# Kernel optimization log

Measured on AMD Instinct MI355X. Metric: run time of the kernel, lower is better.

## Reference

```python
import jax, jax.numpy as jnp
import numpy as np

H, DH = 16, 64            # heads, dim_head (rope dim == DH)
NUM_CHAINS = 2
TWO_PI = 2.0 * np.pi
LN_EPS = 1e-5


def layer_norm(x, gamma):
    mu = jnp.mean(x, axis=-1, keepdims=True)
    var = jnp.var(x, axis=-1, keepdims=True)
    return (x - mu) * jax.lax.rsqrt(var + LN_EPS) * gamma


def rotate_half(x):
    # pairs are interleaved: (..., d*2) viewed as (..., d, 2); (x1,x2)->(-x2,x1)
    x1 = x[..., 0::2]
    x2 = x[..., 1::2]
    return jnp.stack((-x2, x1), axis=-1).reshape(x.shape)


def cyclic_rope_freqs(residue_index, chain_index, cyclic_mask, rope_freqs, dtype):
    """Angles [B,L,DH]: standard RoPE (with chain-offset combination) for linear
    tokens, ring harmonics omega_i = 2*pi*k_i/L_chain for cyclic tokens."""
    t = residue_index.astype(dtype)                      # B L (interpolate_factor=1)
    ci = chain_index.astype(dtype)
    F = rope_freqs.shape[0]                              # DH//2 = 32
    # standard path (RotaryEmbedding._forward with chain_index):
    # residue_indices = arange(F)%F = identity; chain_indices = arange(F)//F = 0
    res = t[..., None] * rope_freqs                      # B L F
    ch0 = ci * rope_freqs[0]                             # B L  (chain_freqs[...,0])
    std = jnp.repeat(res + ch0[..., None], 2, axis=-1)   # B L DH (interleaved repeat)
    # ring size per token: count of cyclic tokens on each token's chain
    oh = jax.nn.one_hot(chain_index, NUM_CHAINS, dtype=dtype)        # B L C
    counts = jnp.einsum('blc,bl->bc', oh, cyclic_mask)               # B C
    ring = jnp.take_along_axis(counts, chain_index, axis=1) * cyclic_mask  # B L
    ring_safe = jnp.maximum(ring, 1.0)
    max_k = jnp.maximum(jnp.floor(ring_safe * 0.5), 1.0)             # B L
    kk = jnp.arange(1, F + 1, dtype=dtype)
    k_eff = jnp.where(max_k[..., None] == 1.0, 1.0,
                      1.0 + jnp.mod(kk - 1.0, max_k[..., None]))     # B L F
    omega = TWO_PI * k_eff / ring_safe[..., None]                    # B L F
    cyc = jnp.repeat(omega * t[..., None], 2, axis=-1)               # B L DH
    return jnp.where((cyclic_mask > 0)[..., None], cyc, std)


def setup_inputs() -> dict:
    key = jax.random.key(0)
    ks = jax.random.split(key, 8)
    B, L, dim = 4, 1024, 1024
    s = 0.02
    x = jax.random.normal(ks[0], (B, L, dim), jnp.float32)
    time = jax.random.normal(ks[1], (B, 1, dim), jnp.float32)
    seq_mask = jnp.ones((B, L), jnp.float32)
    residue_index = (jnp.arange(B * L, dtype=jnp.int32).reshape(B, L)) % L
    chain_index = jax.random.randint(ks[2], (B, L), 0, NUM_CHAINS).astype(jnp.int32)
    cyclic_mask = jax.random.randint(ks[3], (B, L), 0, 2).astype(jnp.float32)
    gamma = jnp.ones((dim,), jnp.float32)
    Wt = jax.random.normal(ks[4], (2 * dim, dim), jnp.float32) * s
    bt = jnp.zeros((2 * dim,), jnp.float32)
    Wq = jax.random.normal(ks[5], (H * DH, dim), jnp.float32) * s
    Wkv = jax.random.normal(ks[6], (2 * H * DH, dim), jnp.float32) * s
    Wo = jax.random.normal(ks[7], (dim, H * DH), jnp.float32) * s
    rope_freqs = 1.0 / (10000.0 ** (jnp.arange(0, DH, 2, dtype=jnp.float32) / DH))
    return {"x": x, "time": time, "seq_mask": seq_mask, "cyclic_mask": cyclic_mask,
            "gamma": gamma, "Wt": Wt, "bt": bt, "Wq": Wq, "Wkv": Wkv, "Wo": Wo,
            "rope_freqs": rope_freqs,
            "residue_index": residue_index, "chain_index": chain_index}


def reference(x, time, seq_mask, cyclic_mask, gamma, Wt, bt, Wq, Wkv, Wo,
              rope_freqs, residue_index, chain_index):
    B, L, dim = x.shape
    x = x * seq_mask[..., None]
    xn = layer_norm(x, gamma)
    # time conditioning: SiLU -> Linear -> (scale, shift)
    ss = jax.nn.silu(time) @ Wt.T + bt                   # B 1 2*dim
    scale, shift = jnp.split(ss, 2, axis=-1)
    xc = xn * (scale + 1.0) + shift                      # B L dim
    q = (xc @ Wq.T).reshape(B, L, H, DH).transpose(0, 2, 1, 3)   # B H L Dh
    k, v = jnp.split(xc @ Wkv.T, 2, axis=-1)
    k = k.reshape(B, L, H, DH).transpose(0, 2, 1, 3)
    v = v.reshape(B, L, H, DH).transpose(0, 2, 1, 3)
    # cyclic rotary embeddings (full head dim rotated)
    freqs = cyclic_rope_freqs(residue_index, chain_index, cyclic_mask,
                              rope_freqs, x.dtype)        # B L DH
    cos_f = jnp.cos(freqs)[:, None]                       # B 1 L DH
    sin_f = jnp.sin(freqs)[:, None]
    q = q * cos_f + rotate_half(q) * sin_f
    k = k * cos_f + rotate_half(k) * sin_f
    sim = jnp.einsum('bhid,bhjd->bhij', q * (DH ** -0.5), k)
    neg = -jnp.finfo(sim.dtype).max
    sim = jnp.where(seq_mask[:, None, None, :] > 0, sim, neg)
    attn = jax.nn.softmax(sim, axis=-1)
    out = jnp.einsum('bhij,bhjd->bhid', attn, v)
    out = out.transpose(0, 2, 1, 3).reshape(B, L, H * DH)
    out = out @ Wo.T
    return out * seq_mask[..., None]
```

## Files before the change

kernel.cpp:

```cpp
#include <hip/hip_runtime.h>
#include <hip/hip_bf16.h>
#include <math.h>

#define NB 4
#define NL 1024
#define NDIM 1024
#define NH 16
#define NDH 64
#define NEG_MAX (-3.402823466e38f)

typedef __attribute__((ext_vector_type(4))) float fx4;
typedef __attribute__((ext_vector_type(8))) short bh8;

__device__ __forceinline__ ushort f2bf(float f){
    __hip_bfloat16 h = __float2bfloat16(f);
    return *(ushort*)&h;
}
__device__ __forceinline__ float bf2f(ushort h){
    return __uint_as_float(((unsigned)h)<<16);
}
__device__ __forceinline__ void gload16(const void* g, void* l){
    __builtin_amdgcn_global_load_lds((const __attribute__((address_space(1))) void*)g,
                                     (__attribute__((address_space(3))) void*)l, 16, 0, 0);
}

__global__ __launch_bounds__(256) void k_ss(const float* __restrict__ time_, const float* __restrict__ Wt,
                                            const float* __restrict__ bt, float* __restrict__ ss){
    int gw   = (blockIdx.x*256 + threadIdx.x) >> 6;
    int lane = threadIdx.x & 63;
    int b = gw >> 11, j = gw & 2047;
    const float* a = time_ + b*NDIM;
    const float* w = Wt + (size_t)j*NDIM;
    float s = 0.f;
    #pragma unroll 4
    for (int i = lane; i < NDIM; i += 64){
        float v = a[i];
        s += (v / (1.f + __expf(-v))) * w[i];
    }
    #pragma unroll
    for (int off=32; off; off>>=1) s += __shfl_xor(s, off, 64);
    if (!lane) ss[gw] = s + bt[j];
}

__global__ __launch_bounds__(256) void k_counts(const int* __restrict__ chain, const float* __restrict__ cyc,
                                                float* __restrict__ counts){
    int b = blockIdx.x >> 1, c = blockIdx.x & 1;
    float s = 0.f;
    for (int l = threadIdx.x; l < NL; l += 256)
        s += (chain[b*NL+l]==c) ? cyc[b*NL+l] : 0.f;
    __shared__ float red[4];
    #pragma unroll
    for (int off=32; off; off>>=1) s += __shfl_xor(s, off, 64);
    if (!(threadIdx.x & 63)) red[threadIdx.x>>6] = s;
    __syncthreads();
    if (!threadIdx.x) counts[blockIdx.x] = red[0]+red[1]+red[2]+red[3];
}

__global__ __launch_bounds__(256) void k_angles(const int* __restrict__ resi, const int* __restrict__ chain,
                                                const float* __restrict__ cyc, const float* __restrict__ rf,
                                                const float* __restrict__ counts,
                                                float* __restrict__ cosb, float* __restrict__ sinb){
    int idx = blockIdx.x*256 + threadIdx.x;
    int f  = idx & 31;
    int bl = idx >> 5;
    int b  = bl >> 10;
    float t  = (float)resi[bl];
    int   ci = chain[bl];
    float cm = cyc[bl];
    float ang;
    if (cm > 0.f) {
        float ring      = counts[b*2+ci] * cm;
        float ring_safe = fmaxf(ring, 1.f);
        float max_k     = fmaxf(floorf(ring_safe*0.5f), 1.f);
        float k_eff     = (max_k == 1.f) ? 1.f : (1.f + fmodf((float)f, max_k));
        float omega     = 6.28318530717958647692f * k_eff / ring_safe;
        ang = omega * t;
    } else {
        ang = t * rf[f] + (float)ci * rf[0];
    }
    cosb[idx] = cosf(ang);
    sinb[idx] = sinf(ang);
}

__global__ __launch_bounds__(256) void k_convall(const float* __restrict__ Wq, const float* __restrict__ Wkv,
                                                 const float* __restrict__ Wo,
                                                 ushort* __restrict__ wqkv, ushort* __restrict__ wo){
    int i = (blockIdx.x*256 + threadIdx.x)*4;
    if (i >= 4194304) return;
    const float* src; ushort* dst;
    if (i < 3145728){
        dst = wqkv + i;
        src = (i < 1048576) ? (Wq + i) : (Wkv + (i - 1048576));
    } else {
        dst = wo + (i - 3145728);
        src = Wo + (i - 3145728);
    }
    fx4 v = *(const fx4*)src;
    ushort4 o; o.x=f2bf(v.x); o.y=f2bf(v.y); o.z=f2bf(v.z); o.w=f2bf(v.w);
    *(ushort4*)dst = o;
}

__global__ __launch_bounds__(256) void k_lnmod(const float* __restrict__ x, const float* __restrict__ sm,
                                               const float* __restrict__ gamma, const float* __restrict__ ss,
                                               ushort* __restrict__ xc){
    int row = blockIdx.x;
    int b   = row >> 10;
    int t   = threadIdx.x;
    float msk = sm[row];
    fx4 v = ((const fx4*)(x + (size_t)row*NDIM))[t];
    v.x*=msk; v.y*=msk; v.z*=msk; v.w*=msk;
    float s1 = v.x+v.y+v.z+v.w;
    float s2 = v.x*v.x + v.y*v.y + v.z*v.z + v.w*v.w;
    __shared__ float r1[4], r2[4];
    #pragma unroll
    for (int off=32; off; off>>=1){ s1 += __shfl_xor(s1,off,64); s2 += __shfl_xor(s2,off,64); }
    if (!(t & 63)){ r1[t>>6]=s1; r2[t>>6]=s2; }
    __syncthreads();
    s1 = r1[0]+r1[1]+r1[2]+r1[3];
    s2 = r2[0]+r2[1]+r2[2]+r2[3];
    float mu  = s1 * (1.f/NDIM);
    float var = s2 * (1.f/NDIM) - mu*mu;
    float rs  = rsqrtf(var + 1e-5f);
    const float* sc = ss + b*2048;
    fx4 g   = ((const fx4*)gamma)[t];
    fx4 scl = ((const fx4*)sc)[t];
    fx4 sh  = ((const fx4*)(sc+1024))[t];
    ushort4 ob;
    ob.x = f2bf((v.x-mu)*rs*g.x*(1.f+scl.x)+sh.x);
    ob.y = f2bf((v.y-mu)*rs*g.y*(1.f+scl.y)+sh.y);
    ob.z = f2bf((v.z-mu)*rs*g.z*(1.f+scl.z)+sh.z);
    ob.w = f2bf((v.w-mu)*rs*g.w*(1.f+scl.w)+sh.w);
    *(ushort4*)(xc + (size_t)row*NDIM + t*4) = ob;
}

template<int MODE>
__global__ __launch_bounds__(256) void k_mm(const ushort* __restrict__ A, const ushort* __restrict__ W,
                                            ushort* __restrict__ qo, ushort* __restrict__ ko,
                                            ushort* __restrict__ vo,
                                            float* __restrict__ outf, const float* __restrict__ smask){
    __shared__ ushort As[128*32];
    __shared__ ushort Bs[128*32];
    int t = threadIdx.x, l = t&63, w = t>>6;
    int lo = l&15, hi = l>>4;
    int m0 = blockIdx.y*128, n0 = blockIdx.x*128;
    int wm = (w>>1)*64, wn = (w&1)*64;
    fx4 acc[4][4];
    #pragma unroll
    for (int i=0;i<4;i++)
        #pragma unroll
        for (int j=0;j<4;j++) acc[i][j] = (fx4){0.f,0.f,0.f,0.f};
    const char* Ab = (const char*)A;
    const char* Wb = (const char*)W;
    for (int k0=0; k0<NDIM; k0+=32){
        __syncthreads();
        #pragma unroll
        for (int e=0;e<2;e++){
            int c = t + e*256;
            int row = c>>2, cw = c&3;
            gload16(Ab + (size_t)(m0+row)*2048 + k0*2 + cw*16, (char*)As + c*16);
            gload16(Wb + (size_t)(n0+row)*2048 + k0*2 + cw*16, (char*)Bs + c*16);
        }
        __syncthreads();
        bh8 af[4], bf[4];
        #pragma unroll
        for (int i=0;i<4;i++) af[i] = *(const bh8*)(As + (wm + i*16 + lo)*32 + hi*8);
        #pragma unroll
        for (int j=0;j<4;j++) bf[j] = *(const bh8*)(Bs + (wn + j*16 + lo)*32 + hi*8);
        #pragma unroll
        for (int i=0;i<4;i++)
            #pragma unroll
            for (int j=0;j<4;j++)
                acc[i][j] = __builtin_amdgcn_mfma_f32_16x16x32_bf16(af[i], bf[j], acc[i][j], 0, 0, 0);
    }
    #pragma unroll
    for (int i=0;i<4;i++){
        #pragma unroll
        for (int r=0;r<4;r++){
            int m = m0 + wm + i*16 + hi*4 + r;
            int b_ = m>>10, l_ = m&1023;
            #pragma unroll
            for (int j=0;j<4;j++){
                int n = n0 + wn + j*16 + lo;
                float val = acc[i][j][r];
                if (MODE==0){
                    int nn = n & 1023;
                    int h_ = nn>>6, d_ = nn&63;
                    size_t off = (size_t)((b_*NH + h_)*NL + l_)*NDH + d_;
                    if (n < 1024)      qo[off] = f2bf(val);
                    else if (n < 2048) ko[off] = f2bf(val);
                    else               vo[off] = f2bf(val);
                } else {
                    outf[(size_t)m*NDIM + n] = val * smask[m];
                }
            }
        }
    }
}

__global__ __launch_bounds__(256) void k_rope(ushort* __restrict__ q, ushort* __restrict__ k,
                                              const float* __restrict__ cosb, const float* __restrict__ sinb){
    int idx = blockIdx.x*256 + threadIdx.x;
    int f   = idx & 31;
    int bhl = idx >> 5;
    int l   = bhl & 1023;
    int b   = bhl >> 14;
    int ca  = ((b<<10)|l)*32 + f;
    float c = cosb[ca], s = sinb[ca];
    const float QS = 0.18033688011112042f;
    unsigned qp = ((const unsigned*)q)[idx];
    unsigned kp = ((const unsigned*)k)[idx];
    float qx = bf2f((ushort)(qp&0xffffu)), qy = bf2f((ushort)(qp>>16));
    float kx = bf2f((ushort)(kp&0xffffu)), ky = bf2f((ushort)(kp>>16));
    float q0 = (qx*c - qy*s)*QS, q1 = (qy*c + qx*s)*QS;
    float k0 = kx*c - ky*s,      k1 = ky*c + kx*s;
    ((unsigned*)q)[idx] = (unsigned)f2bf(q0) | ((unsigned)f2bf(q1)<<16);
    ((unsigned*)k)[idx] = (unsigned)f2bf(k0) | ((unsigned)f2bf(k1)<<16);
}

__global__ __launch_bounds__(256) void k_vt(const ushort* __restrict__ v, ushort* __restrict__ vt){
    __shared__ ushort tile[64][65];
    int t = threadIdx.x;
    int bh = blockIdx.y, l0 = blockIdx.x*64;
    #pragma unroll
    for (int e=0;e<2;e++){
        int c = t + e*256;
        int row = c>>3, cw = c&7;
        bh8 d = *(const bh8*)(v + ((size_t)bh*NL + l0 + row)*NDH + cw*8);
        #pragma unroll
        for (int x=0;x<8;x++) tile[row][cw*8+x] = (ushort)d[x];
    }
    __syncthreads();
    #pragma unroll
    for (int e=0;e<2;e++){
        int c = t + e*256;
        int drow = c>>3, cw = c&7;
        bh8 o;
        #pragma unroll
        for (int x=0;x<8;x++) o[x] = (short)tile[cw*8+x][drow];
        *(bh8*)(vt + ((size_t)bh*NDH + drow)*NL + l0 + cw*8) = o;
    }
}

__global__ __launch_bounds__(256) void k_fattn(const ushort* __restrict__ qb, const ushort* __restrict__ kb,
                                               const ushort* __restrict__ vt, const float* __restrict__ smask,
                                               ushort* __restrict__ ao){
    __shared__ ushort Ks[2][64*64];
    __shared__ ushort Vs[2][64*64];
    __shared__ ushort Ps[4][32*64];
    int t = threadIdx.x, l = t&63, w = t>>6;
    int lo = l&15, hi = l>>4;
    int logical = (blockIdx.x & 7)*64 + (blockIdx.x >> 3);
    int bh = logical >> 3;
    int qt = logical & 7;
    int b = bh>>4, h = bh&15;
    int q0 = qt*128;
    int swzq = (lo&7)<<4;

    bh8 aq[2][2];
    #pragma unroll
    for (int qs=0; qs<2; qs++){
        const ushort* qrow = qb + ((size_t)bh*NL + q0 + w*32 + qs*16 + lo)*NDH;
        aq[qs][0] = *(const bh8*)(qrow + hi*8);
        aq[qs][1] = *(const bh8*)(qrow + 32 + hi*8);
    }
    const float* mrow = smask + b*NL;

    fx4 o[2][4];
    float mrun[2], lrun[2];
    #pragma unroll
    for (int qs=0; qs<2; qs++){
        mrun[qs]=NEG_MAX; lrun[qs]=0.f;
        #pragma unroll
        for (int dt=0; dt<4; dt++) o[qs][dt] = (fx4){0.f,0.f,0.f,0.f};
    }

    const char* kbase = (const char*)(kb + (size_t)bh*NL*NDH);
    const char* vbase = (const char*)(vt + (size_t)bh*NDH*NL);

    #define STAGE(bb, jt) { \
        int j0s = (jt)*64; \
        _Pragma("unroll") \
        for (int e=0;e<2;e++){ \
            int c = t + e*256; \
            int row = c>>3, cw = c&7; \
            int lc = cw ^ (row&7); \
            gload16(kbase + (size_t)(j0s+row)*128 + lc*16, (char*)Ks[bb] + c*16); \
        } \
        _Pragma("unroll") \
        for (int e=0;e<2;e++){ \
            int c = t + e*256; \
            int row = c>>3, cw = c&7; \
            int lc = cw ^ (row&7); \
            gload16(vbase + (size_t)row*2048 + j0s*2 + lc*16, (char*)Vs[bb] + c*16); \
        } }

    STAGE(0, 0);
    __syncthreads();

    for (int tt=0; tt<16; ++tt){
        int cur = tt & 1;
        if (tt < 15) STAGE(cur^1, tt+1);
        int j0 = tt*64;
        const char* KsB = (const char*)Ks[cur];
        const char* VsB = (const char*)Vs[cur];
        char* PsB = (char*)&Ps[w][0];

        bh8 kf[4][2];
        #pragma unroll
        for (int j=0;j<4;j++){
            int row = j*16 + lo;
            int swz = (row&7)<<4;
            kf[j][0] = *(const bh8*)(KsB + row*128 + ((hi*16) ^ swz));
            kf[j][1] = *(const bh8*)(KsB + row*128 + ((64 + hi*16) ^ swz));
        }
        fx4 s[2][4];
        #pragma unroll
        for (int qs=0; qs<2; qs++)
            #pragma unroll
            for (int j=0;j<4;j++){
                fx4 z = (fx4){0.f,0.f,0.f,0.f};
                z = __builtin_amdgcn_mfma_f32_16x16x32_bf16(kf[j][0], aq[qs][0], z, 0,0,0);
                z = __builtin_amdgcn_mfma_f32_16x16x32_bf16(kf[j][1], aq[qs][1], z, 0,0,0);
                s[qs][j] = z;
            }
        #pragma unroll
        for (int j=0;j<4;j++){
            float4 mv = *(const float4*)(mrow + j0 + j*16 + hi*4);
            s[0][j][0] = mv.x>0.f ? s[0][j][0] : NEG_MAX;  s[1][j][0] = mv.x>0.f ? s[1][j][0] : NEG_MAX;
            s[0][j][1] = mv.y>0.f ? s[0][j][1] : NEG_MAX;  s[1][j][1] = mv.y>0.f ? s[1][j][1] : NEG_MAX;
            s[0][j][2] = mv.z>0.f ? s[0][j][2] : NEG_MAX;  s[1][j][2] = mv.z>0.f ? s[1][j][2] : NEG_MAX;
            s[0][j][3] = mv.w>0.f ? s[0][j][3] : NEG_MAX;  s[1][j][3] = mv.w>0.f ? s[1][j][3] : NEG_MAX;
        }

        #pragma unroll
        for (int qs=0; qs<2; qs++){
            float mt = s[qs][0][0];
            #pragma unroll
            for (int j=0;j<4;j++)
                #pragma unroll
                for (int r=0;r<4;r++) mt = fmaxf(mt, s[qs][j][r]);
            mt = fmaxf(mt, __shfl_xor(mt, 16));
            mt = fmaxf(mt, __shfl_xor(mt, 32));
            float mnew = fmaxf(mrun[qs], mt);
            float cc = __builtin_amdgcn_exp2f(mrun[qs] - mnew);
            float p[4][4];
            float rs = 0.f;
            #pragma unroll
            for (int j=0;j<4;j++)
                #pragma unroll
                for (int r=0;r<4;r++){ p[j][r] = __builtin_amdgcn_exp2f(s[qs][j][r] - mnew); rs += p[j][r]; }
            rs += __shfl_xor(rs, 16);
            rs += __shfl_xor(rs, 32);
            lrun[qs] = lrun[qs]*cc + rs;
            mrun[qs] = mnew;
            #pragma unroll
            for (int r=0;r<4;r++){
                float ccr = __shfl(cc, hi*4 + r);
                #pragma unroll
                for (int dt=0; dt<4; dt++) o[qs][dt][r] *= ccr;
            }
            #pragma unroll
            for (int j=0;j<4;j++)
                #pragma unroll
                for (int pp=0; pp<2; pp++){
                    unsigned word = (unsigned)f2bf(p[j][2*pp]) | ((unsigned)f2bf(p[j][2*pp+1])<<16);
                    int kv0 = j*16 + hi*4 + 2*pp;
                    *(unsigned*)(PsB + (qs*16+lo)*128 + ((kv0*2) ^ swzq)) = word;
                }
        }

        bh8 ap[2][2];
        #pragma unroll
        for (int qs=0; qs<2; qs++){
            ap[qs][0] = *(const bh8*)(PsB + (qs*16+lo)*128 + ((hi*16) ^ swzq));
            ap[qs][1] = *(const bh8*)(PsB + (qs*16+lo)*128 + ((64 + hi*16) ^ swzq));
        }
        #pragma unroll
        for (int dt=0; dt<4; dt++){
            int row = dt*16 + lo;
            int swz = (row&7)<<4;
            bh8 bv0 = *(const bh8*)(VsB + row*128 + ((hi*16) ^ swz));
            bh8 bv1 = *(const bh8*)(VsB + row*128 + ((64 + hi*16) ^ swz));
            o[0][dt] = __builtin_amdgcn_mfma_f32_16x16x32_bf16(ap[0][0], bv0, o[0][dt], 0,0,0);
            o[0][dt] = __builtin_amdgcn_mfma_f32_16x16x32_bf16(ap[0][1], bv1, o[0][dt], 0,0,0);
            o[1][dt] = __builtin_amdgcn_mfma_f32_16x16x32_bf16(ap[1][0], bv0, o[1][dt], 0,0,0);
            o[1][dt] = __builtin_amdgcn_mfma_f32_16x16x32_bf16(ap[1][1], bv1, o[1][dt], 0,0,0);
        }
        __syncthreads();
    }
    #undef STAGE

    #pragma unroll
    for (int qs=0; qs<2; qs++){
        float inv = 1.f / lrun[qs];
        #pragma unroll
        for (int r=0;r<4;r++){
            float ivr = __shfl(inv, hi*4 + r);
            int l_ = q0 + w*32 + qs*16 + hi*4 + r;
            size_t base = ((size_t)b*NL + l_)*NDIM + h*NDH;
            #pragma unroll
            for (int dt=0; dt<4; dt++)
                ao[base + dt*16 + lo] = f2bf(o[qs][dt][r] * ivr);
        }
    }
}

extern "C" void kernel_launch(void* const* d_in, const int* in_sizes, int n_in,
                              void* d_out, int out_size, void* d_ws, size_t ws_size,
                              hipStream_t stream) {
    const float* x      = (const float*)d_in[0];
    const float* time_  = (const float*)d_in[1];
    const float* smask  = (const float*)d_in[2];
    const float* cycm   = (const float*)d_in[3];
    const float* gamma  = (const float*)d_in[4];
    const float* Wt     = (const float*)d_in[5];
    const float* bt     = (const float*)d_in[6];
    const float* Wq     = (const float*)d_in[7];
    const float* Wkv    = (const float*)d_in[8];
    const float* Wo     = (const float*)d_in[9];
    const float* rf     = (const float*)d_in[10];
    const int*   resi   = (const int*)d_in[11];
    const int*   chain  = (const int*)d_in[12];
    float* out = (float*)d_out;

    float*  ss     = (float*)d_ws;
    float*  cnts   = ss + 8192;
    float*  cosb   = cnts + 16;
    float*  sinb   = cosb + 131072;
    ushort* xc     = (ushort*)(sinb + 131072);
    ushort* wqkv   = xc + 4194304;
    ushort* wo     = wqkv + 3145728;
    ushort* qbuf   = wo + 1048576;
    ushort* kbuf   = qbuf + 4194304;
    ushort* vbuf   = kbuf + 4194304;
    ushort* vtb    = vbuf + 4194304;
    ushort* aob    = vtb + 4194304;

    hipLaunchKernelGGL(k_ss,      dim3(2048),    dim3(256), 0, stream, time_, Wt, bt, ss);
    hipLaunchKernelGGL(k_counts,  dim3(8),       dim3(256), 0, stream, chain, cycm, cnts);
    hipLaunchKernelGGL(k_angles,  dim3(512),     dim3(256), 0, stream, resi, chain, cycm, rf, cnts, cosb, sinb);
    hipLaunchKernelGGL(k_convall, dim3(4096),    dim3(256), 0, stream, Wq, Wkv, Wo, wqkv, wo);
    hipLaunchKernelGGL(k_lnmod,   dim3(4096),    dim3(256), 0, stream, x, smask, gamma, ss, xc);
    hipLaunchKernelGGL((k_mm<0>), dim3(24,32),   dim3(256), 0, stream, xc, wqkv, qbuf, kbuf, vbuf, (float*)nullptr, (const float*)nullptr);
    hipLaunchKernelGGL(k_rope,    dim3(8192),    dim3(256), 0, stream, qbuf, kbuf, cosb, sinb);
    hipLaunchKernelGGL(k_vt,      dim3(16,64),   dim3(256), 0, stream, vbuf, vtb);
    hipLaunchKernelGGL(k_fattn,   dim3(512),     dim3(256), 0, stream, qbuf, kbuf, vtb, smask, aob);
    hipLaunchKernelGGL((k_mm<1>), dim3(8,32),    dim3(256), 0, stream, aob, wo, (ushort*)nullptr, (ushort*)nullptr, (ushort*)nullptr, out, smask);
}
```

Before: 230.7 us.

## Merge prep kernels, double-buffer GEMM, swizzle tiles, lazy softmax rescale in attention

```diff
diff --git a/kernel.cpp b/kernel.cpp
--- a/kernel.cpp
+++ b/kernel.cpp
@@ -24,113 +24,115 @@
                                      (__attribute__((address_space(3))) void*)l, 16, 0, 0);
 }
 
-__global__ __launch_bounds__(256) void k_ss(const float* __restrict__ time_, const float* __restrict__ Wt,
-                                            const float* __restrict__ bt, float* __restrict__ ss){
-    int gw   = (blockIdx.x*256 + threadIdx.x) >> 6;
-    int lane = threadIdx.x & 63;
-    int b = gw >> 11, j = gw & 2047;
-    const float* a = time_ + b*NDIM;
-    const float* w = Wt + (size_t)j*NDIM;
-    float s = 0.f;
-    #pragma unroll 4
-    for (int i = lane; i < NDIM; i += 64){
-        float v = a[i];
-        s += (v / (1.f + __expf(-v))) * w[i];
-    }
-    #pragma unroll
-    for (int off=32; off; off>>=1) s += __shfl_xor(s, off, 64);
-    if (!lane) ss[gw] = s + bt[j];
-}
-
-__global__ __launch_bounds__(256) void k_counts(const int* __restrict__ chain, const float* __restrict__ cyc,
-                                                float* __restrict__ counts){
-    int b = blockIdx.x >> 1, c = blockIdx.x & 1;
-    float s = 0.f;
-    for (int l = threadIdx.x; l < NL; l += 256)
-        s += (chain[b*NL+l]==c) ? cyc[b*NL+l] : 0.f;
+__global__ __launch_bounds__(256) void k_pre1(const float* __restrict__ time_, const float* __restrict__ Wt,
+                                              const float* __restrict__ bt, float* __restrict__ ss,
+                                              const int* __restrict__ chain, const float* __restrict__ cyc,
+                                              float* __restrict__ counts,
+                                              const float* __restrict__ Wq, const float* __restrict__ Wkv,
+                                              const float* __restrict__ Wo,
+                                              ushort* __restrict__ wqkv, ushort* __restrict__ wo){
     __shared__ float red[4];
-    #pragma unroll
-    for (int off=32; off; off>>=1) s += __shfl_xor(s, off, 64);
-    if (!(threadIdx.x & 63)) red[threadIdx.x>>6] = s;
-    __syncthreads();
-    if (!threadIdx.x) counts[blockIdx.x] = red[0]+red[1]+red[2]+red[3];
-}
-
-__global__ __launch_bounds__(256) void k_angles(const int* __restrict__ resi, const int* __restrict__ chain,
-                                                const float* __restrict__ cyc, const float* __restrict__ rf,
-                                                const float* __restrict__ counts,
-                                                float* __restrict__ cosb, float* __restrict__ sinb){
-    int idx = blockIdx.x*256 + threadIdx.x;
-    int f  = idx & 31;
-    int bl = idx >> 5;
-    int b  = bl >> 10;
-    float t  = (float)resi[bl];
-    int   ci = chain[bl];
-    float cm = cyc[bl];
-    float ang;
-    if (cm > 0.f) {
-        float ring      = counts[b*2+ci] * cm;
-        float ring_safe = fmaxf(ring, 1.f);
-        float max_k     = fmaxf(floorf(ring_safe*0.5f), 1.f);
-        float k_eff     = (max_k == 1.f) ? 1.f : (1.f + fmodf((float)f, max_k));
-        float omega     = 6.28318530717958647692f * k_eff / ring_safe;
-        ang = omega * t;
+    int bx = blockIdx.x, t = threadIdx.x;
+    if (bx < 2048){
+        int gw   = (bx*256 + t) >> 6;
+        int lane = t & 63;
+        int b = gw >> 11, j = gw & 2047;
+        const float* a = time_ + b*NDIM;
+        const float* w = Wt + (size_t)j*NDIM;
+        float s = 0.f;
+        #pragma unroll 4
+        for (int i = lane; i < NDIM; i += 64){
+            float v = a[i];
+            s += (v / (1.f + __expf(-v))) * w[i];
+        }
+        #pragma unroll
+        for (int off=32; off; off>>=1) s += __shfl_xor(s, off, 64);
+        if (!lane) ss[gw] = s + bt[j];
+    } else if (bx < 2056){
+        int cb = bx - 2048;
+        int b = cb >> 1, c = cb & 1;
+        float s = 0.f;
+        for (int l = t; l < NL; l += 256)
+            s += (chain[b*NL+l]==c) ? cyc[b*NL+l] : 0.f;
+        #pragma unroll
+        for (int off=32; off; off>>=1) s += __shfl_xor(s, off, 64);
+        if (!(t & 63)) red[t>>6] = s;
+        __syncthreads();
+        if (!t) counts[cb] = red[0]+red[1]+red[2]+red[3];
     } else {
-        ang = t * rf[f] + (float)ci * rf[0];
-    }
-    cosb[idx] = cosf(ang);
-    sinb[idx] = sinf(ang);
-}
-
-__global__ __launch_bounds__(256) void k_convall(const float* __restrict__ Wq, const float* __restrict__ Wkv,
-                                                 const float* __restrict__ Wo,
-                                                 ushort* __restrict__ wqkv, ushort* __restrict__ wo){
-    int i = (blockIdx.x*256 + threadIdx.x)*4;
-    if (i >= 4194304) return;
-    const float* src; ushort* dst;
-    if (i < 3145728){
-        dst = wqkv + i;
-        src = (i < 1048576) ? (Wq + i) : (Wkv + (i - 1048576));
+        int i = ((bx-2056)*256 + t)*4;
+        const float* src; ushort* dst;
+        if (i < 3145728){
+            dst = wqkv + i;
+            src = (i < 1048576) ? (Wq + i) : (Wkv + (i - 1048576));
+        } else {
+            dst = wo + (i - 3145728);
+            src = Wo + (i - 3145728);
+        }
+        fx4 v = *(const fx4*)src;
+        ushort4 o; o.x=f2bf(v.x); o.y=f2bf(v.y); o.z=f2bf(v.z); o.w=f2bf(v.w);
+        *(ushort4*)dst = o;
+    }
+}
+
+__global__ __launch_bounds__(256) void k_pre2(const int* __restrict__ resi, const int* __restrict__ chain,
+                                              const float* __restrict__ cyc, const float* __restrict__ rf,
+                                              const float* __restrict__ counts,
+                                              float* __restrict__ cosb, float* __restrict__ sinb,
+                                              const float* __restrict__ x, const float* __restrict__ sm,
+                                              const float* __restrict__ gamma, const float* __restrict__ ss,
+                                              ushort* __restrict__ xc){
+    __shared__ float r1[4], r2[4];
+    int bx = blockIdx.x, t = threadIdx.x;
+    if (bx < 512){
+        int idx = bx*256 + t;
+        int f  = idx & 31;
+        int bl = idx >> 5;
+        int b  = bl >> 10;
+        float tt = (float)resi[bl];
+        int   ci = chain[bl];
+        float cm = cyc[bl];
+        float ang;
+        if (cm > 0.f) {
+            float ring      = counts[b*2+ci] * cm;
+            float ring_safe = fmaxf(ring, 1.f);
+            float max_k     = fmaxf(floorf(ring_safe*0.5f), 1.f);
+            float k_eff     = (max_k == 1.f) ? 1.f : (1.f + fmodf((float)f, max_k));
+            float omega     = 6.28318530717958647692f * k_eff / ring_safe;
+            ang = omega * tt;
+        } else {
+            ang = tt * rf[f] + (float)ci * rf[0];
+        }
+        cosb[idx] = cosf(ang);
+        sinb[idx] = sinf(ang);
     } else {
-        dst = wo + (i - 3145728);
-        src = Wo + (i - 3145728);
-    }
-    fx4 v = *(const fx4*)src;
-    ushort4 o; o.x=f2bf(v.x); o.y=f2bf(v.y); o.z=f2bf(v.z); o.w=f2bf(v.w);
-    *(ushort4*)dst = o;
-}
-
-__global__ __launch_bounds__(256) void k_lnmod(const float* __restrict__ x, const float* __restrict__ sm,
-                                               const float* __restrict__ gamma, const float* __restrict__ ss,
-                                               ushort* __restrict__ xc){
-    int row = blockIdx.x;
-    int b   = row >> 10;
-    int t   = threadIdx.x;
-    float msk = sm[row];
-    fx4 v = ((const fx4*)(x + (size_t)row*NDIM))[t];
-    v.x*=msk; v.y*=msk; v.z*=msk; v.w*=msk;
-    float s1 = v.x+v.y+v.z+v.w;
-    float s2 = v.x*v.x + v.y*v.y + v.z*v.z + v.w*v.w;
-    __shared__ float r1[4], r2[4];
-    #pragma unroll
-    for (int off=32; off; off>>=1){ s1 += __shfl_xor(s1,off,64); s2 += __shfl_xor(s2,off,64); }
-    if (!(t & 63)){ r1[t>>6]=s1; r2[t>>6]=s2; }
-    __syncthreads();
-    s1 = r1[0]+r1[1]+r1[2]+r1[3];
-    s2 = r2[0]+r2[1]+r2[2]+r2[3];
-    float mu  = s1 * (1.f/NDIM);
-    float var = s2 * (1.f/NDIM) - mu*mu;
-    float rs  = rsqrtf(var + 1e-5f);
-    const float* sc = ss + b*2048;
-    fx4 g   = ((const fx4*)gamma)[t];
-    fx4 scl = ((const fx4*)sc)[t];
-    fx4 sh  = ((const fx4*)(sc+1024))[t];
-    ushort4 ob;
-    ob.x = f2bf((v.x-mu)*rs*g.x*(1.f+scl.x)+sh.x);
-    ob.y = f2bf((v.y-mu)*rs*g.y*(1.f+scl.y)+sh.y);
-    ob.z = f2bf((v.z-mu)*rs*g.z*(1.f+scl.z)+sh.z);
-    ob.w = f2bf((v.w-mu)*rs*g.w*(1.f+scl.w)+sh.w);
-    *(ushort4*)(xc + (size_t)row*NDIM + t*4) = ob;
+        int row = bx - 512;
+        int b   = row >> 10;
+        float msk = sm[row];
+        fx4 v = ((const fx4*)(x + (size_t)row*NDIM))[t];
+        v.x*=msk; v.y*=msk; v.z*=msk; v.w*=msk;
+        float s1 = v.x+v.y+v.z+v.w;
+        float s2 = v.x*v.x + v.y*v.y + v.z*v.z + v.w*v.w;
+        #pragma unroll
+        for (int off=32; off; off>>=1){ s1 += __shfl_xor(s1,off,64); s2 += __shfl_xor(s2,off,64); }
+        if (!(t & 63)){ r1[t>>6]=s1; r2[t>>6]=s2; }
+        __syncthreads();
+        s1 = r1[0]+r1[1]+r1[2]+r1[3];
+        s2 = r2[0]+r2[1]+r2[2]+r2[3];
+        float mu  = s1 * (1.f/NDIM);
+        float var = s2 * (1.f/NDIM) - mu*mu;
+        float rs  = rsqrtf(var + 1e-5f);
+        const float* sc = ss + b*2048;
+        fx4 g   = ((const fx4*)gamma)[t];
+        fx4 scl = ((const fx4*)sc)[t];
+        fx4 sh  = ((const fx4*)(sc+1024))[t];
+        ushort4 ob;
+        ob.x = f2bf((v.x-mu)*rs*g.x*(1.f+scl.x)+sh.x);
+        ob.y = f2bf((v.y-mu)*rs*g.y*(1.f+scl.y)+sh.y);
+        ob.z = f2bf((v.z-mu)*rs*g.z*(1.f+scl.z)+sh.z);
+        ob.w = f2bf((v.w-mu)*rs*g.w*(1.f+scl.w)+sh.w);
+        *(ushort4*)(xc + (size_t)row*NDIM + t*4) = ob;
+    }
 }
 
 template<int MODE>
@@ -138,11 +140,15 @@
                                             ushort* __restrict__ qo, ushort* __restrict__ ko,
                                             ushort* __restrict__ vo,
                                             float* __restrict__ outf, const float* __restrict__ smask){
-    __shared__ ushort As[128*32];
-    __shared__ ushort Bs[128*32];
+    __shared__ ushort As[2][128*32];
+    __shared__ ushort Bs[2][128*32];
     int t = threadIdx.x, l = t&63, w = t>>6;
     int lo = l&15, hi = l>>4;
-    int m0 = blockIdx.y*128, n0 = blockIdx.x*128;
+    const int nbx = (MODE==0) ? 24 : 8;
+    const int nwg = (MODE==0) ? 768 : 256;
+    int lin = blockIdx.y*nbx + blockIdx.x;
+    int swz = (lin & 7)*(nwg>>3) + (lin>>3);
+    int m0 = (swz/nbx)*128, n0 = (swz%nbx)*128;
     int wm = (w>>1)*64, wn = (w&1)*64;
     fx4 acc[4][4];
     #pragma unroll
@@ -151,27 +157,35 @@
         for (int j=0;j<4;j++) acc[i][j] = (fx4){0.f,0.f,0.f,0.f};
     const char* Ab = (const char*)A;
     const char* Wb = (const char*)W;
-    for (int k0=0; k0<NDIM; k0+=32){
-        __syncthreads();
-        #pragma unroll
-        for (int e=0;e<2;e++){
-            int c = t + e*256;
-            int row = c>>2, cw = c&3;
-            gload16(Ab + (size_t)(m0+row)*2048 + k0*2 + cw*16, (char*)As + c*16);
-            gload16(Wb + (size_t)(n0+row)*2048 + k0*2 + cw*16, (char*)Bs + c*16);
-        }
-        __syncthreads();
+
+    #define MMSTAGE(bb, k0) { \
+        _Pragma("unroll") \
+        for (int e=0;e<2;e++){ \
+            int c = t + e*256; \
+            int row = c>>2, cw = c&3; \
+            gload16(Ab + (size_t)(m0+row)*2048 + (k0)*2 + cw*16, (char*)As[bb] + c*16); \
+            gload16(Wb + (size_t)(n0+row)*2048 + (k0)*2 + cw*16, (char*)Bs[bb] + c*16); \
+        } }
+
+    MMSTAGE(0, 0);
+    __syncthreads();
+    for (int kt=0; kt<32; kt++){
+        int cur = kt & 1;
+        if (kt < 31) MMSTAGE(cur^1, (kt+1)*32);
         bh8 af[4], bf[4];
         #pragma unroll
-        for (int i=0;i<4;i++) af[i] = *(const bh8*)(As + (wm + i*16 + lo)*32 + hi*8);
-        #pragma unroll
-        for (int j=0;j<4;j++) bf[j] = *(const bh8*)(Bs + (wn + j*16 + lo)*32 + hi*8);
+        for (int i=0;i<4;i++) af[i] = *(const bh8*)(&As[cur][0] + (wm + i*16 + lo)*32 + hi*8);
+        #pragma unroll
+        for (int j=0;j<4;j++) bf[j] = *(const bh8*)(&Bs[cur][0] + (wn + j*16 + lo)*32 + hi*8);
         #pragma unroll
         for (int i=0;i<4;i++)
             #pragma unroll
             for (int j=0;j<4;j++)
                 acc[i][j] = __builtin_amdgcn_mfma_f32_16x16x32_bf16(af[i], bf[j], acc[i][j], 0, 0, 0);
-    }
+        __syncthreads();
+    }
+    #undef MMSTAGE
+
     #pragma unroll
     for (int i=0;i<4;i++){
         #pragma unroll
@@ -197,47 +211,49 @@
     }
 }
 
-__global__ __launch_bounds__(256) void k_rope(ushort* __restrict__ q, ushort* __restrict__ k,
-                                              const float* __restrict__ cosb, const float* __restrict__ sinb){
-    int idx = blockIdx.x*256 + threadIdx.x;
-    int f   = idx & 31;
-    int bhl = idx >> 5;
-    int l   = bhl & 1023;
-    int b   = bhl >> 14;
-    int ca  = ((b<<10)|l)*32 + f;
-    float c = cosb[ca], s = sinb[ca];
-    const float QS = 0.18033688011112042f;
-    unsigned qp = ((const unsigned*)q)[idx];
-    unsigned kp = ((const unsigned*)k)[idx];
-    float qx = bf2f((ushort)(qp&0xffffu)), qy = bf2f((ushort)(qp>>16));
-    float kx = bf2f((ushort)(kp&0xffffu)), ky = bf2f((ushort)(kp>>16));
-    float q0 = (qx*c - qy*s)*QS, q1 = (qy*c + qx*s)*QS;
-    float k0 = kx*c - ky*s,      k1 = ky*c + kx*s;
-    ((unsigned*)q)[idx] = (unsigned)f2bf(q0) | ((unsigned)f2bf(q1)<<16);
-    ((unsigned*)k)[idx] = (unsigned)f2bf(k0) | ((unsigned)f2bf(k1)<<16);
-}
-
-__global__ __launch_bounds__(256) void k_vt(const ushort* __restrict__ v, ushort* __restrict__ vt){
+__global__ __launch_bounds__(256) void k_mid(ushort* __restrict__ q, ushort* __restrict__ k,
+                                             const float* __restrict__ cosb, const float* __restrict__ sinb,
+                                             const ushort* __restrict__ v, ushort* __restrict__ vt){
     __shared__ ushort tile[64][65];
-    int t = threadIdx.x;
-    int bh = blockIdx.y, l0 = blockIdx.x*64;
-    #pragma unroll
-    for (int e=0;e<2;e++){
-        int c = t + e*256;
-        int row = c>>3, cw = c&7;
-        bh8 d = *(const bh8*)(v + ((size_t)bh*NL + l0 + row)*NDH + cw*8);
-        #pragma unroll
-        for (int x=0;x<8;x++) tile[row][cw*8+x] = (ushort)d[x];
-    }
-    __syncthreads();
-    #pragma unroll
-    for (int e=0;e<2;e++){
-        int c = t + e*256;
-        int drow = c>>3, cw = c&7;
-        bh8 o;
-        #pragma unroll
-        for (int x=0;x<8;x++) o[x] = (short)tile[cw*8+x][drow];
-        *(bh8*)(vt + ((size_t)bh*NDH + drow)*NL + l0 + cw*8) = o;
+    int bx = blockIdx.x, t = threadIdx.x;
+    if (bx < 8192){
+        int idx = bx*256 + t;
+        int f   = idx & 31;
+        int bhl = idx >> 5;
+        int l   = bhl & 1023;
+        int b   = bhl >> 14;
+        int ca  = ((b<<10)|l)*32 + f;
+        float c = cosb[ca], s = sinb[ca];
+        const float QS = 0.18033688011112042f;
+        unsigned qp = ((const unsigned*)q)[idx];
+        unsigned kp = ((const unsigned*)k)[idx];
+        float qx = bf2f((ushort)(qp&0xffffu)), qy = bf2f((ushort)(qp>>16));
+        float kx = bf2f((ushort)(kp&0xffffu)), ky = bf2f((ushort)(kp>>16));
+        float q0 = (qx*c - qy*s)*QS, q1 = (qy*c + qx*s)*QS;
+        float k0 = kx*c - ky*s,      k1 = ky*c + kx*s;
+        ((unsigned*)q)[idx] = (unsigned)f2bf(q0) | ((unsigned)f2bf(q1)<<16);
+        ((unsigned*)k)[idx] = (unsigned)f2bf(k0) | ((unsigned)f2bf(k1)<<16);
+    } else {
+        int vb = bx - 8192;
+        int bh = vb >> 4, l0 = (vb & 15)*64;
+        #pragma unroll
+        for (int e=0;e<2;e++){
+            int c = t + e*256;
+            int row = c>>3, cw = c&7;
+            bh8 d = *(const bh8*)(v + ((size_t)bh*NL + l0 + row)*NDH + cw*8);
+            #pragma unroll
+            for (int x2=0;x2<8;x2++) tile[row][cw*8+x2] = (ushort)d[x2];
+        }
+        __syncthreads();
+        #pragma unroll
+        for (int e=0;e<2;e++){
+            int c = t + e*256;
+            int drow = c>>3, cw = c&7;
+            bh8 o;
+            #pragma unroll
+            for (int x2=0;x2<8;x2++) o[x2] = (short)tile[cw*8+x2][drow];
+            *(bh8*)(vt + ((size_t)bh*NDH + drow)*NL + l0 + cw*8) = o;
+        }
     }
 }
 
@@ -314,6 +330,7 @@
             kf[j][1] = *(const bh8*)(KsB + row*128 + ((64 + hi*16) ^ swz));
         }
         fx4 s[2][4];
+        __builtin_amdgcn_s_setprio(1);
         #pragma unroll
         for (int qs=0; qs<2; qs++)
             #pragma unroll
@@ -323,6 +340,7 @@
                 z = __builtin_amdgcn_mfma_f32_16x16x32_bf16(kf[j][1], aq[qs][1], z, 0,0,0);
                 s[qs][j] = z;
             }
+        __builtin_amdgcn_s_setprio(0);
         #pragma unroll
         for (int j=0;j<4;j++){
             float4 mv = *(const float4*)(mrow + j0 + j*16 + hi*4);
@@ -334,39 +352,46 @@
 
         #pragma unroll
         for (int qs=0; qs<2; qs++){
-            float mt = s[qs][0][0];
+            float m0 = fmaxf(fmaxf(s[qs][0][0], s[qs][0][1]), s[qs][0][2]);
+            float m1 = fmaxf(fmaxf(s[qs][0][3], s[qs][1][0]), s[qs][1][1]);
+            float m2 = fmaxf(fmaxf(s[qs][1][2], s[qs][1][3]), s[qs][2][0]);
+            float m3 = fmaxf(fmaxf(s[qs][2][1], s[qs][2][2]), s[qs][2][3]);
+            float m4 = fmaxf(fmaxf(s[qs][3][0], s[qs][3][1]), s[qs][3][2]);
+            float mt = fmaxf(fmaxf(fmaxf(m0,m1),m2), fmaxf(fmaxf(m3,m4), s[qs][3][3]));
+            mt = fmaxf(mt, __shfl_xor(mt, 16));
+            mt = fmaxf(mt, __shfl_xor(mt, 32));
+            if (__any(mt > mrun[qs] + 8.f)){
+                float mnew = fmaxf(mrun[qs], mt);
+                float cc = __builtin_amdgcn_exp2f(mrun[qs] - mnew);
+                lrun[qs] *= cc;
+                mrun[qs] = mnew;
+                #pragma unroll
+                for (int r=0;r<4;r++){
+                    float ccr = __shfl(cc, hi*4 + r);
+                    #pragma unroll
+                    for (int dt=0; dt<4; dt++) o[qs][dt][r] *= ccr;
+                }
+            }
+            float p[4][4];
             #pragma unroll
             for (int j=0;j<4;j++)
                 #pragma unroll
-                for (int r=0;r<4;r++) mt = fmaxf(mt, s[qs][j][r]);
-            mt = fmaxf(mt, __shfl_xor(mt, 16));
-            mt = fmaxf(mt, __shfl_xor(mt, 32));
-            float mnew = fmaxf(mrun[qs], mt);
-            float cc = __builtin_amdgcn_exp2f(mrun[qs] - mnew);
-            float p[4][4];
-            float rs = 0.f;
-            #pragma unroll
-            for (int j=0;j<4;j++)
-                #pragma unroll
-                for (int r=0;r<4;r++){ p[j][r] = __builtin_amdgcn_exp2f(s[qs][j][r] - mnew); rs += p[j][r]; }
+                for (int r=0;r<4;r++) p[j][r] = __builtin_amdgcn_exp2f(s[qs][j][r] - mrun[qs]);
+            float r0 = (p[0][0]+p[0][1]) + (p[0][2]+p[0][3]);
+            float r1 = (p[1][0]+p[1][1]) + (p[1][2]+p[1][3]);
+            float r2 = (p[2][0]+p[2][1]) + (p[2][2]+p[2][3]);
+            float r3 = (p[3][0]+p[3][1]) + (p[3][2]+p[3][3]);
+            float rs = (r0+r1)+(r2+r3);
             rs += __shfl_xor(rs, 16);
             rs += __shfl_xor(rs, 32);
-            lrun[qs] = lrun[qs]*cc + rs;
-            mrun[qs] = mnew;
-            #pragma unroll
-            for (int r=0;r<4;r++){
-                float ccr = __shfl(cc, hi*4 + r);
-                #pragma unroll
-                for (int dt=0; dt<4; dt++) o[qs][dt][r] *= ccr;
+            lrun[qs] += rs;
+            #pragma unroll
+            for (int j=0;j<4;j++){
+                uint2 wd;
+                wd.x = (unsigned)f2bf(p[j][0]) | ((unsigned)f2bf(p[j][1])<<16);
+                wd.y = (unsigned)f2bf(p[j][2]) | ((unsigned)f2bf(p[j][3])<<16);
+                *(uint2*)(PsB + (qs*16+lo)*128 + ((j*32 + hi*8) ^ swzq)) = wd;
             }
-            #pragma unroll
-            for (int j=0;j<4;j++)
-                #pragma unroll
-                for (int pp=0; pp<2; pp++){
-                    unsigned word = (unsigned)f2bf(p[j][2*pp]) | ((unsigned)f2bf(p[j][2*pp+1])<<16);
-                    int kv0 = j*16 + hi*4 + 2*pp;
-                    *(unsigned*)(PsB + (qs*16+lo)*128 + ((kv0*2) ^ swzq)) = word;
-                }
         }
 
         bh8 ap[2][2];
@@ -375,6 +400,7 @@
             ap[qs][0] = *(const bh8*)(PsB + (qs*16+lo)*128 + ((hi*16) ^ swzq));
             ap[qs][1] = *(const bh8*)(PsB + (qs*16+lo)*128 + ((64 + hi*16) ^ swzq));
         }
+        __builtin_amdgcn_s_setprio(1);
         #pragma unroll
         for (int dt=0; dt<4; dt++){
             int row = dt*16 + lo;
@@ -386,6 +412,7 @@
             o[1][dt] = __builtin_amdgcn_mfma_f32_16x16x32_bf16(ap[1][0], bv0, o[1][dt], 0,0,0);
             o[1][dt] = __builtin_amdgcn_mfma_f32_16x16x32_bf16(ap[1][1], bv1, o[1][dt], 0,0,0);
         }
+        __builtin_amdgcn_s_setprio(0);
         __syncthreads();
     }
     #undef STAGE
@@ -436,14 +463,16 @@
     ushort* vtb    = vbuf + 4194304;
     ushort* aob    = vtb + 4194304;
 
-    hipLaunchKernelGGL(k_ss,      dim3(2048),    dim3(256), 0, stream, time_, Wt, bt, ss);
-    hipLaunchKernelGGL(k_counts,  dim3(8),       dim3(256), 0, stream, chain, cycm, cnts);
-    hipLaunchKernelGGL(k_angles,  dim3(512),     dim3(256), 0, stream, resi, chain, cycm, rf, cnts, cosb, sinb);
-    hipLaunchKernelGGL(k_convall, dim3(4096),    dim3(256), 0, stream, Wq, Wkv, Wo, wqkv, wo);
-    hipLaunchKernelGGL(k_lnmod,   dim3(4096),    dim3(256), 0, stream, x, smask, gamma, ss, xc);
-    hipLaunchKernelGGL((k_mm<0>), dim3(24,32),   dim3(256), 0, stream, xc, wqkv, qbuf, kbuf, vbuf, (float*)nullptr, (const float*)nullptr);
-    hipLaunchKernelGGL(k_rope,    dim3(8192),    dim3(256), 0, stream, qbuf, kbuf, cosb, sinb);
-    hipLaunchKernelGGL(k_vt,      dim3(16,64),   dim3(256), 0, stream, vbuf, vtb);
-    hipLaunchKernelGGL(k_fattn,   dim3(512),     dim3(256), 0, stream, qbuf, kbuf, vtb, smask, aob);
-    hipLaunchKernelGGL((k_mm<1>), dim3(8,32),    dim3(256), 0, stream, aob, wo, (ushort*)nullptr, (ushort*)nullptr, (ushort*)nullptr, out, smask);
-}
+    hipLaunchKernelGGL(k_pre1,   dim3(6152),   dim3(256), 0, stream,
+                       time_, Wt, bt, ss, chain, cycm, cnts, Wq, Wkv, Wo, wqkv, wo);
+    hipLaunchKernelGGL(k_pre2,   dim3(4608),   dim3(256), 0, stream,
+                       resi, chain, cycm, rf, cnts, cosb, sinb, x, smask, gamma, ss, xc);
+    hipLaunchKernelGGL((k_mm<0>), dim3(24,32), dim3(256), 0, stream,
+                       xc, wqkv, qbuf, kbuf, vbuf, (float*)nullptr, (const float*)nullptr);
+    hipLaunchKernelGGL(k_mid,    dim3(9216),   dim3(256), 0, stream,
+                       qbuf, kbuf, cosb, sinb, vbuf, vtb);
+    hipLaunchKernelGGL(k_fattn,  dim3(512),    dim3(256), 0, stream,
+                       qbuf, kbuf, vtb, smask, aob);
+    hipLaunchKernelGGL((k_mm<1>), dim3(8,32),  dim3(256), 0, stream,
+                       aob, wo, (ushort*)nullptr, (ushort*)nullptr, (ushort*)nullptr, out, smask);
+}
```

New measurement: 220.2 us. 1.05x faster.
